# Kernel tuning notes

Measured on AMD Instinct MI355X. Metric: run time of the kernel, lower is better.

Reference implementation:

```python
import jax, jax.numpy as jnp
import numpy as np

B, C, H, W = 64, 256, 32, 32


def setup_inputs() -> dict:
    key = jax.random.key(0)
    ks = jax.random.split(key, 7)
    x1 = jax.random.normal(ks[0], (B, C, H, W), dtype=jnp.float32)
    x2 = jax.random.normal(ks[1], (B, C, H, W), dtype=jnp.float32)
    # 1x1 Conv2d(C+1 -> C, bias=False): weight squeezed to (C, C+1)
    conv_w = jax.random.normal(ks[2], (C, C + 1), dtype=jnp.float32) * (1.0 / np.sqrt(C + 1))
    # caLayer: Conv1d(2->4, k=1) + ReLU + Conv1d(4->1, k=1) + Softmax(dim=1)
    ca_w1 = jax.random.normal(ks[3], (4, 2), dtype=jnp.float32) * (1.0 / np.sqrt(2))
    ca_b1 = jax.random.normal(ks[4], (4,), dtype=jnp.float32) * 0.1
    ca_w2 = jax.random.normal(ks[5], (1, 4), dtype=jnp.float32) * 0.5
    ca_b2 = jax.random.normal(ks[6], (1,), dtype=jnp.float32) * 0.1
    return {"x1": x1, "x2": x2, "conv_w": conv_w, "ca_w1": ca_w1,
            "ca_b1": ca_b1, "ca_w2": ca_w2, "ca_b2": ca_b2}


def _branch_pool(x, conv_w):
    # x: (B, C, H, W)
    b, c, h, w = x.shape
    center = x[:, :, h // 2, w // 2][:, :, None, None]          # (B, C, 1, 1)
    dot = jnp.sum(x * center, axis=1, keepdims=True) / c        # (B, 1, H, W)
    concatenated = jnp.concatenate([x, dot], axis=1)            # (B, C+1, H, W)
    attn = jax.nn.sigmoid(jnp.einsum('oc,bchw->bohw', conv_w, concatenated))
    norm = attn / (jnp.sum(attn, axis=(2, 3), keepdims=True) + 1e-8)
    return jnp.sum(x * norm, axis=(2, 3))                       # (B, C)


def reference(x1, x2, conv_w, ca_w1, ca_b1, ca_w2, ca_b2):
    pooled = jnp.stack([_branch_pool(x1, conv_w),
                        _branch_pool(x2, conv_w)], axis=1)      # (B, 2, C)
    # caLayer: kernel-size-1 Conv1d == channel-mixing matmul over axis 1
    h1 = jax.nn.relu(jnp.einsum('oi,bic->boc', ca_w1, pooled) + ca_b1[None, :, None])
    h2 = jnp.einsum('oi,bic->boc', ca_w2, h1) + ca_b2[None, :, None]  # (B, 1, C)
    x_weights = jax.nn.softmax(h2, axis=1)                      # softmax over size-1 dim
    y_total = pooled * x_weights                                # broadcast (B,2,C)
    return jnp.sum(y_total, axis=1)                             # (B, C)
```

## Files before the change

### kernel.cpp

```cpp
#include <hip/hip_runtime.h>
#include <hip/hip_bf16.h>
#include <math.h>

typedef __bf16 bf16x8 __attribute__((ext_vector_type(8)));
typedef float  f32x16 __attribute__((ext_vector_type(16)));

#define WLAST_OFF 32768
#define CEN_OFF   33024
#define ACCA_OFF  65792
#define ACCX_OFF  98560

static __device__ __forceinline__ unsigned f2bf_u(float f) {
    unsigned u = __builtin_bit_cast(unsigned, f);
    return (u + 0x7fffu + ((u >> 16) & 1u)) >> 16;
}
static __device__ __forceinline__ unsigned pkbf(float a, float b) {
    __hip_bfloat162 h = __float22bfloat162_rn(make_float2(a, b));
    unsigned u; __builtin_memcpy(&u, &h, 4); return u;
}

template<int CTRL, int RM>
static __device__ __forceinline__ float dpp_add(float x) {
    int yi = __builtin_amdgcn_update_dpp(0, __builtin_bit_cast(int, x), CTRL, RM, 0xF, true);
    return x + __builtin_bit_cast(float, yi);
}
static __device__ __forceinline__ float red32(float x) {
    x = dpp_add<0x121, 0xF>(x);
    x = dpp_add<0x122, 0xF>(x);
    x = dpp_add<0x124, 0xF>(x);
    x = dpp_add<0x128, 0xF>(x);
    x = dpp_add<0x142, 0xA>(x);
    return x;
}

__global__ void k_init(const float* __restrict__ x1, const float* __restrict__ x2,
                       const float* __restrict__ conv_w, float* __restrict__ ws) {
    int bk = blockIdx.x;
    int tid = threadIdx.x;
    if (bk < 256) {
        int idx = bk * 256 + tid;
        int j  = idx & 7;
        int l  = (idx >> 3) & 63;
        int ot = (idx >> 9) & 7;
        int S  = idx >> 12;
        int o  = ot * 32 + (l & 31);
        int k  = S * 16 + (l >> 5) * 8 + j;
        ((unsigned short*)ws)[idx] = (unsigned short)f2bf_u(conv_w[o * 257 + k]);
        if (idx < 256) ws[WLAST_OFF + idx] = conv_w[idx * 257 + 256];
        ws[ACCA_OFF + idx] = 0.0f;
    } else {
        int xb = bk - 256;
        const float* xp = ((xb < 64) ? x1 : x2) + (size_t)(xb & 63) * (256 * 1024);
        ws[CEN_OFF + xb * 256 + tid] = xp[(size_t)tid * 1024 + 528];
    }
}

__global__ __launch_bounds__(512, 4)
void k_main(const float* __restrict__ x1, const float* __restrict__ x2,
            float* __restrict__ ws) {
    int bx = blockIdx.x;
    int xb = blockIdx.y;
    const float* xp = ((xb < 64) ? x1 : x2) + (size_t)(xb & 63) * (256 * 1024);
    const unsigned short* wfrag = (const unsigned short*)ws;
    float* accA = ws + ACCA_OFF + xb * 256;
    float* accX = ws + ACCX_OFF + xb * 256;
    int hw0 = bx * 64;

    int tid = threadIdx.x;
    int w = tid >> 6;
    int l = tid & 63;
    int lw = l & 31, q = l >> 5;

    __shared__ __align__(16) unsigned sx[16][64][8];
    __shared__ float sd[64][9];
    __shared__ float swl[256];
    __shared__ float dotf[64];

    int hwi = tid & 15, kc = tid >> 4;

    if (tid < 256) swl[tid] = ws[WLAST_OFF + tid];

    const float* cenp = ws + CEN_OFF + xb * 256;
    float2 cv[4];
    #pragma unroll
    for (int s = 0; s < 4; ++s)
        cv[s] = *(const float2*)(cenp + kc * 2 + 64 * s);
    const float* xst = xp + (size_t)(kc * 2) * 1024 + hw0 + hwi * 4;
    float4 xv[8];
    #pragma unroll
    for (int s = 0; s < 4; ++s) {
        xv[2 * s]     = *(const float4*)(xst + (size_t)(64 * s) * 1024);
        xv[2 * s + 1] = *(const float4*)(xst + (size_t)(64 * s + 1) * 1024);
    }
    const unsigned short* ap = wfrag + (size_t)(w * 64 + l) * 8;
    bf16x8 A[16];
    #pragma unroll
    for (int S = 0; S < 16; ++S)
        A[S] = *(const bf16x8*)(ap + (size_t)S * 4096);
    __builtin_amdgcn_sched_barrier(0);

    float dotp[4] = {0.f, 0.f, 0.f, 0.f};
    #pragma unroll
    for (int s = 0; s < 4; ++s) {
        float4 e = xv[2 * s], o4 = xv[2 * s + 1];
        float s0 = cv[s].x, s1 = cv[s].y;
        dotp[0] += e.x * s0 + o4.x * s1;
        dotp[1] += e.y * s0 + o4.y * s1;
        dotp[2] += e.z * s0 + o4.z * s1;
        dotp[3] += e.w * s0 + o4.w * s1;
        int S  = (kc >> 3) + 4 * s;
        int wd = kc & 7;
        float ee[4] = {e.x, e.y, e.z, e.w};
        float oo[4] = {o4.x, o4.y, o4.z, o4.w};
        #pragma unroll
        for (int j = 0; j < 4; ++j) {
            int jj  = (hwi + j) & 3;
            int hwr = hwi * 4 + jj;
            sx[S][hwr][wd ^ (((hwr >> 4) & 1) << 2)] = pkbf(ee[jj], oo[jj]);
        }
    }
    #pragma unroll
    for (int j = 0; j < 4; ++j) {
        float v = dotp[j];
        v += __shfl_xor(v, 16, 64);
        v += __shfl_xor(v, 32, 64);
        dotp[j] = v;
    }
    if (l < 16) {
        #pragma unroll
        for (int j = 0; j < 4; ++j) sd[hwi * 4 + j][w] = dotp[j];
    }
    __syncthreads();

    if (tid < 64) {
        float ssum = 0.f;
        #pragma unroll
        for (int k2 = 0; k2 < 8; ++k2) ssum += sd[tid][k2];
        dotf[tid] = ssum * (1.0f / 256.0f);
    }

    f32x16 acc[2];
    #pragma unroll
    for (int e = 0; e < 16; ++e) { acc[0][e] = 0.0f; acc[1][e] = 0.0f; }

    int sig = ((lw >> 4) & 1) << 2;
    const unsigned* b0p = &sx[0][lw][(q * 4) ^ sig];
    const unsigned* b1p = &sx[0][32 + lw][(q * 4) ^ sig];

    #pragma unroll
    for (int S = 0; S < 16; ++S) {
        bf16x8 b0, b1;
        __builtin_memcpy(&b0, b0p + S * 512, 16);
        __builtin_memcpy(&b1, b1p + S * 512, 16);
        acc[0] = __builtin_amdgcn_mfma_f32_32x32x16_bf16(A[S], b0, acc[0], 0, 0, 0);
        acc[1] = __builtin_amdgcn_mfma_f32_32x32x16_bf16(A[S], b1, acc[1], 0, 0, 0);
    }
    __syncthreads();

    float dv0 = dotf[lw];
    float dv1 = dotf[32 + lw];
    #pragma unroll
    for (int r = 0; r < 16; ++r) {
        int row = (r & 3) + 8 * (r >> 2) + 4 * q;
        int o = w * 32 + row;
        float wl = swl[o];
        float z0 = acc[0][r] + wl * dv0;
        float z1 = acc[1][r] + wl * dv1;
        float a0s = __builtin_amdgcn_rcpf(1.0f + __expf(-z0));
        float a1s = __builtin_amdgcn_rcpf(1.0f + __expf(-z1));
        int Si = o >> 4, wd = (o >> 1) & 7;
        unsigned w0 = sx[Si][lw][wd ^ sig];
        unsigned w1 = sx[Si][32 + lw][wd ^ sig];
        float xv0, xv1;
        if (o & 1) {
            xv0 = __builtin_bit_cast(float, w0 & 0xffff0000u);
            xv1 = __builtin_bit_cast(float, w1 & 0xffff0000u);
        } else {
            xv0 = __builtin_bit_cast(float, w0 << 16);
            xv1 = __builtin_bit_cast(float, w1 << 16);
        }
        float sA = red32(a0s + a1s);
        float sX = red32(a0s * xv0 + a1s * xv1);
        if (lw == 31) {
            atomicAdd(&accA[o], sA);
            atomicAdd(&accX[o], sX);
        }
    }
}

__global__ void k_out(const float* __restrict__ ws, float* __restrict__ out) {
    int idx = blockIdx.x * 256 + threadIdx.x;
    int b = idx >> 8, o = idx & 255;
    float a0 = ws[ACCA_OFF + b * 256 + o];
    float p0 = ws[ACCX_OFF + b * 256 + o];
    float a1 = ws[ACCA_OFF + (64 + b) * 256 + o];
    float p1 = ws[ACCX_OFF + (64 + b) * 256 + o];
    out[idx] = p0 / (a0 + 1e-8f) + p1 / (a1 + 1e-8f);
}

extern "C" void kernel_launch(void* const* d_in, const int* in_sizes, int n_in,
                              void* d_out, int out_size, void* d_ws, size_t ws_size,
                              hipStream_t stream) {
    const float* x1     = (const float*)d_in[0];
    const float* x2     = (const float*)d_in[1];
    const float* conv_w = (const float*)d_in[2];
    float* ws  = (float*)d_ws;
    float* out = (float*)d_out;

    k_init<<<384, 256, 0, stream>>>(x1, x2, conv_w, ws);
    k_main<<<dim3(16, 128), 512, 0, stream>>>(x1, x2, ws);
    k_out<<<64, 256, 0, stream>>>(ws, out);
}
```

Before: 178.0 us.

## Make k_main persistent over eight HW tiles with register prefetch and accumulation

```diff
diff --git a/kernel.cpp b/kernel.cpp
--- a/kernel.cpp
+++ b/kernel.cpp
@@ -6,7 +6,6 @@
 typedef float  f32x16 __attribute__((ext_vector_type(16)));
 
 #define WLAST_OFF 32768
-#define CEN_OFF   33024
 #define ACCA_OFF  65792
 #define ACCX_OFF  98560
 
@@ -17,6 +16,10 @@
 static __device__ __forceinline__ unsigned pkbf(float a, float b) {
     __hip_bfloat162 h = __float22bfloat162_rn(make_float2(a, b));
     unsigned u; __builtin_memcpy(&u, &h, 4); return u;
+}
+
+static __device__ __forceinline__ void barrier_lds() {
+    asm volatile("s_waitcnt lgkmcnt(0)\n\ts_barrier" ::: "memory");
 }
 
 template<int CTRL, int RM>
@@ -33,38 +36,31 @@
     return x;
 }
 
-__global__ void k_init(const float* __restrict__ x1, const float* __restrict__ x2,
-                       const float* __restrict__ conv_w, float* __restrict__ ws) {
+__global__ void k_init(const float* __restrict__ conv_w, float* __restrict__ ws) {
     int bk = blockIdx.x;
     int tid = threadIdx.x;
-    if (bk < 256) {
-        int idx = bk * 256 + tid;
-        int j  = idx & 7;
-        int l  = (idx >> 3) & 63;
-        int ot = (idx >> 9) & 7;
-        int S  = idx >> 12;
-        int o  = ot * 32 + (l & 31);
-        int k  = S * 16 + (l >> 5) * 8 + j;
-        ((unsigned short*)ws)[idx] = (unsigned short)f2bf_u(conv_w[o * 257 + k]);
-        if (idx < 256) ws[WLAST_OFF + idx] = conv_w[idx * 257 + 256];
-        ws[ACCA_OFF + idx] = 0.0f;
-    } else {
-        int xb = bk - 256;
-        const float* xp = ((xb < 64) ? x1 : x2) + (size_t)(xb & 63) * (256 * 1024);
-        ws[CEN_OFF + xb * 256 + tid] = xp[(size_t)tid * 1024 + 528];
-    }
-}
-
-__global__ __launch_bounds__(512, 4)
+    int idx = bk * 256 + tid;
+    int j  = idx & 7;
+    int l  = (idx >> 3) & 63;
+    int ot = (idx >> 9) & 7;
+    int S  = idx >> 12;
+    int o  = ot * 32 + (l & 31);
+    int k  = S * 16 + (l >> 5) * 8 + j;
+    ((unsigned short*)ws)[idx] = (unsigned short)f2bf_u(conv_w[o * 257 + k]);
+    if (idx < 256) ws[WLAST_OFF + idx] = conv_w[idx * 257 + 256];
+    ws[ACCA_OFF + idx] = 0.0f;
+}
+
+__global__ __launch_bounds__(512, 2)
 void k_main(const float* __restrict__ x1, const float* __restrict__ x2,
             float* __restrict__ ws) {
     int bx = blockIdx.x;
-    int xb = blockIdx.y;
-    const float* xp = ((xb < 64) ? x1 : x2) + (size_t)(xb & 63) * (256 * 1024);
+    int xb = bx >> 1;
+    int half = bx & 1;
+    const float* xpi = ((xb < 64) ? x1 : x2) + (size_t)(xb & 63) * (256 * 1024);
     const unsigned short* wfrag = (const unsigned short*)ws;
     float* accA = ws + ACCA_OFF + xb * 256;
     float* accX = ws + ACCX_OFF + xb * 256;
-    int hw0 = bx * 64;
 
     int tid = threadIdx.x;
     int w = tid >> 6;
@@ -74,116 +70,142 @@
     __shared__ __align__(16) unsigned sx[16][64][8];
     __shared__ float sd[64][9];
     __shared__ float swl[256];
+    __shared__ float scen[256];
     __shared__ float dotf[64];
 
     int hwi = tid & 15, kc = tid >> 4;
 
-    if (tid < 256) swl[tid] = ws[WLAST_OFF + tid];
-
-    const float* cenp = ws + CEN_OFF + xb * 256;
-    float2 cv[4];
-    #pragma unroll
-    for (int s = 0; s < 4; ++s)
-        cv[s] = *(const float2*)(cenp + kc * 2 + 64 * s);
-    const float* xst = xp + (size_t)(kc * 2) * 1024 + hw0 + hwi * 4;
-    float4 xv[8];
-    #pragma unroll
-    for (int s = 0; s < 4; ++s) {
-        xv[2 * s]     = *(const float4*)(xst + (size_t)(64 * s) * 1024);
-        xv[2 * s + 1] = *(const float4*)(xst + (size_t)(64 * s + 1) * 1024);
+    float cenv = 0.f, wlv = 0.f;
+    if (tid < 256) {
+        cenv = xpi[(size_t)tid * 1024 + 528];
+        wlv  = ws[WLAST_OFF + tid];
     }
     const unsigned short* ap = wfrag + (size_t)(w * 64 + l) * 8;
     bf16x8 A[16];
     #pragma unroll
     for (int S = 0; S < 16; ++S)
         A[S] = *(const bf16x8*)(ap + (size_t)S * 4096);
-    __builtin_amdgcn_sched_barrier(0);
-
-    float dotp[4] = {0.f, 0.f, 0.f, 0.f};
+
+    const float* xbase = xpi + half * 512 + (size_t)(kc * 2) * 1024 + hwi * 4;
+    float4 xv[8];
     #pragma unroll
     for (int s = 0; s < 4; ++s) {
-        float4 e = xv[2 * s], o4 = xv[2 * s + 1];
-        float s0 = cv[s].x, s1 = cv[s].y;
-        dotp[0] += e.x * s0 + o4.x * s1;
-        dotp[1] += e.y * s0 + o4.y * s1;
-        dotp[2] += e.z * s0 + o4.z * s1;
-        dotp[3] += e.w * s0 + o4.w * s1;
-        int S  = (kc >> 3) + 4 * s;
-        int wd = kc & 7;
-        float ee[4] = {e.x, e.y, e.z, e.w};
-        float oo[4] = {o4.x, o4.y, o4.z, o4.w};
-        #pragma unroll
-        for (int j = 0; j < 4; ++j) {
-            int jj  = (hwi + j) & 3;
-            int hwr = hwi * 4 + jj;
-            sx[S][hwr][wd ^ (((hwr >> 4) & 1) << 2)] = pkbf(ee[jj], oo[jj]);
-        }
-    }
-    #pragma unroll
-    for (int j = 0; j < 4; ++j) {
-        float v = dotp[j];
-        v += __shfl_xor(v, 16, 64);
-        v += __shfl_xor(v, 32, 64);
-        dotp[j] = v;
-    }
-    if (l < 16) {
-        #pragma unroll
-        for (int j = 0; j < 4; ++j) sd[hwi * 4 + j][w] = dotp[j];
-    }
-    __syncthreads();
-
-    if (tid < 64) {
-        float ssum = 0.f;
-        #pragma unroll
-        for (int k2 = 0; k2 < 8; ++k2) ssum += sd[tid][k2];
-        dotf[tid] = ssum * (1.0f / 256.0f);
-    }
-
-    f32x16 acc[2];
-    #pragma unroll
-    for (int e = 0; e < 16; ++e) { acc[0][e] = 0.0f; acc[1][e] = 0.0f; }
+        xv[2 * s]     = *(const float4*)(xbase + (size_t)(64 * s) * 1024);
+        xv[2 * s + 1] = *(const float4*)(xbase + (size_t)(64 * s + 1) * 1024);
+    }
+    if (tid < 256) { scen[tid] = cenv; swl[tid] = wlv; }
+    barrier_lds();
 
     int sig = ((lw >> 4) & 1) << 2;
     const unsigned* b0p = &sx[0][lw][(q * 4) ^ sig];
     const unsigned* b1p = &sx[0][32 + lw][(q * 4) ^ sig];
 
-    #pragma unroll
-    for (int S = 0; S < 16; ++S) {
-        bf16x8 b0, b1;
-        __builtin_memcpy(&b0, b0p + S * 512, 16);
-        __builtin_memcpy(&b1, b1p + S * 512, 16);
-        acc[0] = __builtin_amdgcn_mfma_f32_32x32x16_bf16(A[S], b0, acc[0], 0, 0, 0);
-        acc[1] = __builtin_amdgcn_mfma_f32_32x32x16_bf16(A[S], b1, acc[1], 0, 0, 0);
-    }
-    __syncthreads();
-
-    float dv0 = dotf[lw];
-    float dv1 = dotf[32 + lw];
+    float sA[16], sX[16];
+    #pragma unroll
+    for (int r = 0; r < 16; ++r) { sA[r] = 0.f; sX[r] = 0.f; }
+
+    #pragma unroll 1
+    for (int t = 0; t < 8; ++t) {
+        if (t) barrier_lds();
+
+        float dotp[4] = {0.f, 0.f, 0.f, 0.f};
+        #pragma unroll
+        for (int s = 0; s < 4; ++s) {
+            float4 e = xv[2 * s], o4 = xv[2 * s + 1];
+            int c = kc * 2 + 64 * s;
+            float s0 = scen[c], s1 = scen[c + 1];
+            dotp[0] += e.x * s0 + o4.x * s1;
+            dotp[1] += e.y * s0 + o4.y * s1;
+            dotp[2] += e.z * s0 + o4.z * s1;
+            dotp[3] += e.w * s0 + o4.w * s1;
+            int S  = (kc >> 3) + 4 * s;
+            int wd = kc & 7;
+            float ee[4] = {e.x, e.y, e.z, e.w};
+            float oo[4] = {o4.x, o4.y, o4.z, o4.w};
+            #pragma unroll
+            for (int j = 0; j < 4; ++j) {
+                int jj  = (hwi + j) & 3;
+                int hwr = hwi * 4 + jj;
+                sx[S][hwr][wd ^ (((hwr >> 4) & 1) << 2)] = pkbf(ee[jj], oo[jj]);
+            }
+        }
+        if (t < 7) {
+            const float* xn = xbase + (t + 1) * 64;
+            #pragma unroll
+            for (int s = 0; s < 4; ++s) {
+                xv[2 * s]     = *(const float4*)(xn + (size_t)(64 * s) * 1024);
+                xv[2 * s + 1] = *(const float4*)(xn + (size_t)(64 * s + 1) * 1024);
+            }
+        }
+        #pragma unroll
+        for (int j = 0; j < 4; ++j) {
+            float v = dotp[j];
+            v += __shfl_xor(v, 16, 64);
+            v += __shfl_xor(v, 32, 64);
+            dotp[j] = v;
+        }
+        if (l < 16) {
+            #pragma unroll
+            for (int j = 0; j < 4; ++j) sd[hwi * 4 + j][w] = dotp[j];
+        }
+        barrier_lds();
+
+        if (tid < 64) {
+            float ssum = 0.f;
+            #pragma unroll
+            for (int k2 = 0; k2 < 8; ++k2) ssum += sd[tid][k2];
+            dotf[tid] = ssum * (1.0f / 256.0f);
+        }
+
+        f32x16 acc0, acc1;
+        #pragma unroll
+        for (int e = 0; e < 16; ++e) { acc0[e] = 0.0f; acc1[e] = 0.0f; }
+        #pragma unroll
+        for (int S = 0; S < 16; ++S) {
+            bf16x8 b0, b1;
+            __builtin_memcpy(&b0, b0p + S * 512, 16);
+            __builtin_memcpy(&b1, b1p + S * 512, 16);
+            acc0 = __builtin_amdgcn_mfma_f32_32x32x16_bf16(A[S], b0, acc0, 0, 0, 0);
+            acc1 = __builtin_amdgcn_mfma_f32_32x32x16_bf16(A[S], b1, acc1, 0, 0, 0);
+        }
+        barrier_lds();
+
+        float dv0 = dotf[lw];
+        float dv1 = dotf[32 + lw];
+        #pragma unroll
+        for (int r = 0; r < 16; ++r) {
+            int row = (r & 3) + 8 * (r >> 2) + 4 * q;
+            int o = w * 32 + row;
+            float wl = swl[o];
+            float z0 = acc0[r] + wl * dv0;
+            float z1 = acc1[r] + wl * dv1;
+            float a0s = __builtin_amdgcn_rcpf(1.0f + __expf(-z0));
+            float a1s = __builtin_amdgcn_rcpf(1.0f + __expf(-z1));
+            int Si = o >> 4, wd = (o >> 1) & 7;
+            unsigned w0 = sx[Si][lw][wd ^ sig];
+            unsigned w1 = sx[Si][32 + lw][wd ^ sig];
+            float xv0, xv1;
+            if (o & 1) {
+                xv0 = __builtin_bit_cast(float, w0 & 0xffff0000u);
+                xv1 = __builtin_bit_cast(float, w1 & 0xffff0000u);
+            } else {
+                xv0 = __builtin_bit_cast(float, w0 << 16);
+                xv1 = __builtin_bit_cast(float, w1 << 16);
+            }
+            sA[r] += a0s + a1s;
+            sX[r] += a0s * xv0 + a1s * xv1;
+        }
+    }
+
     #pragma unroll
     for (int r = 0; r < 16; ++r) {
         int row = (r & 3) + 8 * (r >> 2) + 4 * q;
         int o = w * 32 + row;
-        float wl = swl[o];
-        float z0 = acc[0][r] + wl * dv0;
-        float z1 = acc[1][r] + wl * dv1;
-        float a0s = __builtin_amdgcn_rcpf(1.0f + __expf(-z0));
-        float a1s = __builtin_amdgcn_rcpf(1.0f + __expf(-z1));
-        int Si = o >> 4, wd = (o >> 1) & 7;
-        unsigned w0 = sx[Si][lw][wd ^ sig];
-        unsigned w1 = sx[Si][32 + lw][wd ^ sig];
-        float xv0, xv1;
-        if (o & 1) {
-            xv0 = __builtin_bit_cast(float, w0 & 0xffff0000u);
-            xv1 = __builtin_bit_cast(float, w1 & 0xffff0000u);
-        } else {
-            xv0 = __builtin_bit_cast(float, w0 << 16);
-            xv1 = __builtin_bit_cast(float, w1 << 16);
-        }
-        float sA = red32(a0s + a1s);
-        float sX = red32(a0s * xv0 + a1s * xv1);
+        float rA = red32(sA[r]);
+        float rX = red32(sX[r]);
         if (lw == 31) {
-            atomicAdd(&accA[o], sA);
-            atomicAdd(&accX[o], sX);
+            atomicAdd(&accA[o], rA);
+            atomicAdd(&accX[o], rX);
         }
     }
 }
@@ -207,7 +229,7 @@
     float* ws  = (float*)d_ws;
     float* out = (float*)d_out;
 
-    k_init<<<384, 256, 0, stream>>>(x1, x2, conv_w, ws);
-    k_main<<<dim3(16, 128), 512, 0, stream>>>(x1, x2, ws);
+    k_init<<<256, 256, 0, stream>>>(conv_w, ws);
+    k_main<<<256, 512, 0, stream>>>(x1, x2, ws);
     k_out<<<64, 256, 0, stream>>>(ws, out);
 }
```

After: 163.9 us. 1.09x faster.
